# Kernel tuning notes

Measured on AMD Instinct MI355X. Metric: run time of the kernel, lower is better.

## Reference

```python
import jax, jax.numpy as jnp
import numpy as np

CODEBOOK_SIZE = 8192
EMBED_DIM = 128
BETA = 0.25


def setup_inputs() -> dict:
    key = jax.random.key(0)
    k1, k2, k3, k4 = jax.random.split(key, 4)
    z = jax.random.normal(k1, (8, 4096, EMBED_DIM), dtype=jnp.float32)
    # nn.Embedding init: normal(0, D**-0.5), frozen
    emb_weight = jax.random.normal(k2, (CODEBOOK_SIZE, EMBED_DIM), dtype=jnp.float32) * (EMBED_DIM ** -0.5)
    # nn.Linear default init scale ~ 1/sqrt(in_features)
    lim = 1.0 / np.sqrt(EMBED_DIM)
    proj_w = jax.random.uniform(k3, (EMBED_DIM, EMBED_DIM), jnp.float32, -lim, lim)
    proj_b = jax.random.uniform(k4, (EMBED_DIM,), jnp.float32, -lim, lim)
    return {"z": z, "emb_weight": emb_weight, "proj_w": proj_w, "proj_b": proj_b}


def reference(z, emb_weight, proj_w, proj_b):
    z_flat = z.reshape(-1, EMBED_DIM)  # [T, D]
    # embedding_proj: Linear -> codebook @ W^T + b
    quant_codebook = emb_weight @ proj_w.T + proj_b  # [K, D]
    # squared distances: |z|^2 + |c|^2 - 2 z c^T  -> [T, K]
    d = (jnp.sum(z_flat ** 2, axis=1, keepdims=True)
         + jnp.sum(quant_codebook ** 2, axis=1)
         - 2.0 * jnp.einsum('td,kd->tk', z_flat, quant_codebook))
    idx = jnp.argmin(d, axis=1)  # [T]
    z_q = quant_codebook[idx].reshape(z.shape)
    # codebook usage / perplexity
    counts = jax.ops.segment_sum(jnp.ones_like(idx, dtype=jnp.float32), idx,
                                 num_segments=CODEBOOK_SIZE)
    e_mean = counts / idx.shape[0]
    perplexity = jnp.exp(-jnp.sum(e_mean * jnp.log(e_mean + 1e-8)))
    sg = jax.lax.stop_gradient
    commit_loss = (BETA * jnp.mean((sg(z_q) - z) ** 2)
                   + jnp.mean((z_q - sg(z)) ** 2))
    z_q_st = z + sg(z_q - z)  # straight-through estimator
    return (z_q_st, commit_loss, perplexity)
```

## Files before the change

kernel.cpp:

```cpp
#include <hip/hip_runtime.h>
#include <math.h>

#define T_TOK 32768
#define D_DIM 128
#define K_CODE 8192
#define BM 256
#define BN 64

typedef unsigned long long ull;
typedef _Float16 v8h __attribute__((ext_vector_type(8)));
typedef _Float16 v4h __attribute__((ext_vector_type(4)));
typedef float v16f __attribute__((ext_vector_type(16)));

#define SCALE 4096.0f
#define DESCALE (1.0f / 4096.0f)
#define ACC_SCALE (-0x1p-23f)


__global__ __launch_bounds__(64) void proj_kernel(const float* __restrict__ E,
                                                  const float* __restrict__ W,
                                                  const float* __restrict__ b,
                                                  char* __restrict__ Cpack,
                                                  float* __restrict__ cn) {
    int r = blockIdx.x;
    int l = threadIdx.x;
    const float4* E4 = (const float4*)(E + (size_t)r * D_DIM);
    const float4* WA = (const float4*)(W + (size_t)l * D_DIM);
    const float4* WB = (const float4*)(W + (size_t)(l + 64) * D_DIM);

    float4 aA = make_float4(0.f, 0.f, 0.f, 0.f);
    float4 aB = make_float4(0.f, 0.f, 0.f, 0.f);
#pragma unroll
    for (int dd = 0; dd < 32; ++dd) {
        float4 e = E4[dd];
        float4 wa = WA[dd], wb = WB[dd];
        aA.x = fmaf(e.x, wa.x, aA.x);
        aA.y = fmaf(e.y, wa.y, aA.y);
        aA.z = fmaf(e.z, wa.z, aA.z);
        aA.w = fmaf(e.w, wa.w, aA.w);
        aB.x = fmaf(e.x, wb.x, aB.x);
        aB.y = fmaf(e.y, wb.y, aB.y);
        aB.z = fmaf(e.z, wb.z, aB.z);
        aB.w = fmaf(e.w, wb.w, aB.w);
    }
    float vA = ((aA.x + aA.y) + (aA.z + aA.w)) + b[l];
    float vB = ((aB.x + aB.y) + (aB.z + aB.w)) + b[l + 64];

    char* cp = Cpack + (size_t)(r >> 6) * 32768;
    int mt = (r >> 5) & 1, rs = r & 31;
    {
        int kc = l >> 4, hf = (l >> 3) & 1, j = l & 7;
        float f = vA * SCALE;
        _Float16 h = (_Float16)f;
        _Float16 m = (_Float16)(f - (float)h);
        size_t off = (size_t)((mt * 8 + kc) * 1024 + (hf * 32 + rs) * 16 + j * 2);
        *(_Float16*)(cp + off) = h;
        *(_Float16*)(cp + off + 16384) = m;
    }
    {
        int d = l + 64;
        int kc = d >> 4, hf = (d >> 3) & 1, j = d & 7;
        float f = vB * SCALE;
        _Float16 h = (_Float16)f;
        _Float16 m = (_Float16)(f - (float)h);
        size_t off = (size_t)((mt * 8 + kc) * 1024 + (hf * 32 + rs) * 16 + j * 2);
        *(_Float16*)(cp + off) = h;
        *(_Float16*)(cp + off + 16384) = m;
    }

    float s = vA * vA + vB * vB;
#pragma unroll
    for (int off = 32; off > 0; off >>= 1) s += __shfl_down(s, off, 64);
    if (l == 0) cn[r] = s;
}

__global__ __launch_bounds__(64) void znorm_kernel(const float* __restrict__ Z,
                                                   float* __restrict__ zn,
                                                   ull* __restrict__ packed,
                                                   int* __restrict__ counts,
                                                   float* __restrict__ loss) {
    int t = blockIdx.x;
    int l = threadIdx.x;
    float a = Z[(size_t)t * D_DIM + l];
    float b2 = Z[(size_t)t * D_DIM + 64 + l];
    float s = a * a + b2 * b2;
#pragma unroll
    for (int off = 32; off > 0; off >>= 1) s += __shfl_down(s, off, 64);
    if (l == 0) {
        zn[t] = s;
        packed[t] = ~0ull;
        if (t < K_CODE) counts[t] = 0;
        if (t == 0) loss[0] = 0.f;
    }
}

__global__ __launch_bounds__(256) void prep_z_kernel(const float* __restrict__ Z,
                                                     char* __restrict__ Zpack) {
    int tb = blockIdx.x;
    int tid = threadIdx.x;
    int lane = tid & 63;
    int w = tid >> 6;
    char* zp = Zpack + (size_t)tb * 16384;
#pragma unroll
    for (int kq = 0; kq < 2; ++kq) {
        int kc = 2 * w + kq;
        const float* src = Z + (size_t)(tb * 32 + (lane & 31)) * D_DIM
                             + kc * 16 + (lane >> 5) * 8;
        float4 a = *(const float4*)(src);
        float4 c = *(const float4*)(src + 4);
        float vals[8] = {a.x, a.y, a.z, a.w, c.x, c.y, c.z, c.w};
        v8h h, m;
#pragma unroll
        for (int j = 0; j < 8; ++j) {
            float f = vals[j] * SCALE;
            _Float16 hh = (_Float16)f;
            h[j] = hh;
            m[j] = (_Float16)(f - (float)hh);
        }
        *(v8h*)(zp + (size_t)(kc * 1024 + lane * 16)) = h;
        *(v8h*)(zp + (size_t)(8192 + kc * 1024 + lane * 16)) = m;
    }
}

__global__ __launch_bounds__(256, 3) void argmin_kernel(const char* __restrict__ Zpack,
                                                        const char* __restrict__ Cpack,
                                                        const float* __restrict__ cn,
                                                        const float* __restrict__ zn,
                                                        ull* __restrict__ packed) {
    __shared__ char lds[33024];

    int tid = threadIdx.x;
    int lane = tid & 63;
    int w = __builtin_amdgcn_readfirstlane(tid >> 6);
    int cb = blockIdx.x;
    int nb = cb * BN;
    int mb = blockIdx.y * BM;

    {
        const float4* src = (const float4*)(Cpack + (size_t)cb * 32768);
        float4* dst = (float4*)lds;
#pragma unroll
        for (int it = 0; it < 8; ++it) dst[it * 256 + tid] = src[it * 256 + tid];
        if (tid < 64) *(float*)(lds + 32768 + tid * 4) = cn[nb + tid];
    }
    __syncthreads();

    v16f acc[2][2];
#pragma unroll
    for (int mt = 0; mt < 2; ++mt)
#pragma unroll
        for (int nt = 0; nt < 2; ++nt) acc[mt][nt] = (v16f)0.f;

    int tb0 = (mb >> 5) + 2 * w;
    const char* zb00 = Zpack + (size_t)tb0 * 16384 + lane * 16;
    const char* zb01 = zb00 + 8192;
    const char* zb10 = Zpack + (size_t)(tb0 + 1) * 16384 + lane * 16;
    const char* zb11 = zb10 + 8192;
    const char* ab = lds + lane * 16;

    v8h pBh0 = *(const v8h*)(zb00);
    v8h pBm0 = *(const v8h*)(zb01);
    v8h pBh1 = *(const v8h*)(zb10);
    v8h pBm1 = *(const v8h*)(zb11);

#pragma unroll
    for (int kc = 0; kc < 8; ++kc) {
        v8h Bh0 = pBh0, Bm0 = pBm0, Bh1 = pBh1, Bm1 = pBm1;
        if (kc < 7) {
            pBh0 = *(const v8h*)(zb00 + (kc + 1) * 1024);
            pBm0 = *(const v8h*)(zb01 + (kc + 1) * 1024);
            pBh1 = *(const v8h*)(zb10 + (kc + 1) * 1024);
            pBm1 = *(const v8h*)(zb11 + (kc + 1) * 1024);
        }
        v8h Ah0 = *(const v8h*)(ab + (0 * 8 + kc) * 1024);
        v8h Ah1 = *(const v8h*)(ab + (1 * 8 + kc) * 1024);
        v8h Am0 = *(const v8h*)(ab + (2 * 8 + kc) * 1024);
        v8h Am1 = *(const v8h*)(ab + (3 * 8 + kc) * 1024);

        acc[0][0] = __builtin_amdgcn_mfma_f32_32x32x16_f16(Ah0, Bh0, acc[0][0], 0, 0, 0);
        acc[0][1] = __builtin_amdgcn_mfma_f32_32x32x16_f16(Ah0, Bh1, acc[0][1], 0, 0, 0);
        acc[1][0] = __builtin_amdgcn_mfma_f32_32x32x16_f16(Ah1, Bh0, acc[1][0], 0, 0, 0);
        acc[1][1] = __builtin_amdgcn_mfma_f32_32x32x16_f16(Ah1, Bh1, acc[1][1], 0, 0, 0);
        acc[0][0] = __builtin_amdgcn_mfma_f32_32x32x16_f16(Ah0, Bm0, acc[0][0], 0, 0, 0);
        acc[0][1] = __builtin_amdgcn_mfma_f32_32x32x16_f16(Ah0, Bm1, acc[0][1], 0, 0, 0);
        acc[1][0] = __builtin_amdgcn_mfma_f32_32x32x16_f16(Ah1, Bm0, acc[1][0], 0, 0, 0);
        acc[1][1] = __builtin_amdgcn_mfma_f32_32x32x16_f16(Ah1, Bm1, acc[1][1], 0, 0, 0);
        acc[0][0] = __builtin_amdgcn_mfma_f32_32x32x16_f16(Am0, Bh0, acc[0][0], 0, 0, 0);
        acc[0][1] = __builtin_amdgcn_mfma_f32_32x32x16_f16(Am0, Bh1, acc[0][1], 0, 0, 0);
        acc[1][0] = __builtin_amdgcn_mfma_f32_32x32x16_f16(Am1, Bh0, acc[1][0], 0, 0, 0);
        acc[1][1] = __builtin_amdgcn_mfma_f32_32x32x16_f16(Am1, Bh1, acc[1][1], 0, 0, 0);
    }

    const float* cn_s = (const float*)(lds + 32768);
    int half_id = lane >> 5;
    int tok0 = mb + w * 64 + (lane & 31);
    int tok1 = tok0 + 32;
    float zn0 = zn[tok0], zn1 = zn[tok1];

    float best0 = 3.4e38f, best1 = 3.4e38f;
    int bi0 = nb, bi1 = nb;
#pragma unroll
    for (int mt = 0; mt < 2; ++mt) {
#pragma unroll
        for (int reg = 0; reg < 16; ++reg) {
            int mrow = 32 * mt + (reg & 3) + 8 * (reg >> 2) + 4 * half_id;
            float cnv = cn_s[mrow];
            int code = nb + mrow;
            float s0 = fmaf(acc[mt][0][reg], ACC_SCALE, zn0 + cnv);
            float s1 = fmaf(acc[mt][1][reg], ACC_SCALE, zn1 + cnv);
            if (s0 < best0) { best0 = s0; bi0 = code; }
            if (s1 < best1) { best1 = s1; bi1 = code; }
        }
    }
    {
        float ob = __shfl_xor(best0, 32, 64);
        int oi = __shfl_xor(bi0, 32, 64);
        if (ob < best0 || (ob == best0 && oi < bi0)) { best0 = ob; bi0 = oi; }
        ob = __shfl_xor(best1, 32, 64);
        oi = __shfl_xor(bi1, 32, 64);
        if (ob < best1 || (ob == best1 && oi < bi1)) { best1 = ob; bi1 = oi; }
    }
    if (half_id == 0) {
        ull pk = ((ull)__float_as_uint(best0) << 32) | (unsigned)bi0;
        atomicMin(&packed[tok0], pk);
    } else {
        ull pk = ((ull)__float_as_uint(best1) << 32) | (unsigned)bi1;
        atomicMin(&packed[tok1], pk);
    }
}

__global__ __launch_bounds__(256) void zq_kernel(const float* __restrict__ Z,
                                                 const char* __restrict__ Cpack,
                                                 const ull* __restrict__ packed,
                                                 float* __restrict__ out,
                                                 int* __restrict__ counts,
                                                 float* __restrict__ loss) {
    int gid = blockIdx.x * 256 + threadIdx.x;
    int t = gid >> 5;
    int d4 = gid & 31;
    int idx = (int)(packed[t] & 0xFFFFFFFFull);
    if (d4 == 0) atomicAdd(&counts[idx], 1);

    int d0 = 4 * d4;
    int kc = d0 >> 4, hf = (d0 >> 3) & 1, j0 = d0 & 7;
    const char* cp = Cpack + (size_t)(idx >> 6) * 32768
                   + (size_t)((((idx >> 5) & 1) * 8 + kc) * 1024
                              + (hf * 32 + (idx & 31)) * 16 + j0 * 2);
    v4h h = *(const v4h*)(cp);
    v4h m = *(const v4h*)(cp + 16384);
    float4 cv;
    cv.x = ((float)h[0] + (float)m[0]) * DESCALE;
    cv.y = ((float)h[1] + (float)m[1]) * DESCALE;
    cv.z = ((float)h[2] + (float)m[2]) * DESCALE;
    cv.w = ((float)h[3] + (float)m[3]) * DESCALE;

    float4 zv = ((const float4*)Z)[gid];
    float dx = cv.x - zv.x, dy = cv.y - zv.y, dz = cv.z - zv.z, dw = cv.w - zv.w;
    float4 o;
    o.x = zv.x + dx;
    o.y = zv.y + dy;
    o.z = zv.z + dz;
    o.w = zv.w + dw;
    ((float4*)out)[gid] = o;

    float ls = dx * dx + dy * dy + dz * dz + dw * dw;
#pragma unroll
    for (int off = 32; off > 0; off >>= 1) ls += __shfl_down(ls, off, 64);
    __shared__ float red[4];
    int lane = threadIdx.x & 63, w = threadIdx.x >> 6;
    if (lane == 0) red[w] = ls;
    __syncthreads();
    if (threadIdx.x == 0) {
        atomicAdd(loss, (red[0] + red[1]) + (red[2] + red[3]));
    }
}

__global__ __launch_bounds__(256) void scalars_kernel(const int* __restrict__ counts,
                                                      const float* __restrict__ loss,
                                                      float* __restrict__ out) {
    float s = 0.f;
    for (int i = threadIdx.x; i < K_CODE; i += 256) {
        float e = (float)counts[i] * (1.0f / (float)T_TOK);
        s += e * logf(e + 1e-8f);
    }
#pragma unroll
    for (int off = 32; off > 0; off >>= 1) s += __shfl_down(s, off, 64);
    __shared__ float red[4];
    int lane = threadIdx.x & 63, w = threadIdx.x >> 6;
    if (lane == 0) red[w] = s;
    __syncthreads();
    if (threadIdx.x == 0) {
        float ssum = (red[0] + red[1]) + (red[2] + red[3]);
        out[(size_t)T_TOK * D_DIM + 0] = 1.25f * loss[0] / (float)((size_t)T_TOK * D_DIM);
        out[(size_t)T_TOK * D_DIM + 1] = expf(-ssum);
    }
}

extern "C" void kernel_launch(void* const* d_in, const int* in_sizes, int n_in,
                              void* d_out, int out_size, void* d_ws, size_t ws_size,
                              hipStream_t stream) {
    const float* z   = (const float*)d_in[0];
    const float* emb = (const float*)d_in[1];
    const float* pw  = (const float*)d_in[2];
    const float* pb  = (const float*)d_in[3];
    float* out = (float*)d_out;

    char* Zpack = (char*)d_out;

    char* ws = (char*)d_ws;
    char*  Cpack  = ws + 0;
    float* cn     = (float*)(ws + 4194304);
    float* zn     = (float*)(ws + 4227072);
    ull*   packed = (ull*)  (ws + 4358144);
    int*   counts = (int*)  (ws + 4620288);
    float* loss   = (float*)(ws + 4653056);

    proj_kernel<<<K_CODE, 64, 0, stream>>>(emb, pw, pb, Cpack, cn);
    prep_z_kernel<<<T_TOK / 32, 256, 0, stream>>>(z, Zpack);
    znorm_kernel<<<T_TOK, 64, 0, stream>>>(z, zn, packed, counts, loss);
    argmin_kernel<<<dim3(K_CODE / BN, T_TOK / BM), 256, 0, stream>>>(Zpack, Cpack, cn, zn, packed);
    zq_kernel<<<(T_TOK * D_DIM / 4) / 256, 256, 0, stream>>>(z, Cpack, packed, out, counts, loss);
    scalars_kernel<<<1, 256, 0, stream>>>(counts, loss, out);
}
```

Measured before the change: 419.9 us.

## Fuse prep kernels into one launch and double-buffer argmin operand loads

Merges the codebook projection, Z packing and Z norm/init kernels into a single prep launch split by block index, removing two kernel launches and their gaps. The argmin kernel now uses two-deep register rings, fetching B from global two k-steps ahead and prefetching A from LDS one step ahead. This is meant to hide global and LDS load latency behind the MFMAs, at the cost of more VGPRs, which could reduce occupancy under the 3-block launch bound.

```diff
diff --git a/kernel.cpp b/kernel.cpp
--- a/kernel.cpp
+++ b/kernel.cpp
@@ -17,108 +17,110 @@
 #define ACC_SCALE (-0x1p-23f)
 
 
-__global__ __launch_bounds__(64) void proj_kernel(const float* __restrict__ E,
-                                                  const float* __restrict__ W,
-                                                  const float* __restrict__ b,
-                                                  char* __restrict__ Cpack,
-                                                  float* __restrict__ cn) {
-    int r = blockIdx.x;
-    int l = threadIdx.x;
-    const float4* E4 = (const float4*)(E + (size_t)r * D_DIM);
-    const float4* WA = (const float4*)(W + (size_t)l * D_DIM);
-    const float4* WB = (const float4*)(W + (size_t)(l + 64) * D_DIM);
-
-    float4 aA = make_float4(0.f, 0.f, 0.f, 0.f);
-    float4 aB = make_float4(0.f, 0.f, 0.f, 0.f);
-#pragma unroll
-    for (int dd = 0; dd < 32; ++dd) {
-        float4 e = E4[dd];
-        float4 wa = WA[dd], wb = WB[dd];
-        aA.x = fmaf(e.x, wa.x, aA.x);
-        aA.y = fmaf(e.y, wa.y, aA.y);
-        aA.z = fmaf(e.z, wa.z, aA.z);
-        aA.w = fmaf(e.w, wa.w, aA.w);
-        aB.x = fmaf(e.x, wb.x, aB.x);
-        aB.y = fmaf(e.y, wb.y, aB.y);
-        aB.z = fmaf(e.z, wb.z, aB.z);
-        aB.w = fmaf(e.w, wb.w, aB.w);
-    }
-    float vA = ((aA.x + aA.y) + (aA.z + aA.w)) + b[l];
-    float vB = ((aB.x + aB.y) + (aB.z + aB.w)) + b[l + 64];
-
-    char* cp = Cpack + (size_t)(r >> 6) * 32768;
-    int mt = (r >> 5) & 1, rs = r & 31;
-    {
-        int kc = l >> 4, hf = (l >> 3) & 1, j = l & 7;
-        float f = vA * SCALE;
-        _Float16 h = (_Float16)f;
-        _Float16 m = (_Float16)(f - (float)h);
-        size_t off = (size_t)((mt * 8 + kc) * 1024 + (hf * 32 + rs) * 16 + j * 2);
-        *(_Float16*)(cp + off) = h;
-        *(_Float16*)(cp + off + 16384) = m;
-    }
-    {
-        int d = l + 64;
-        int kc = d >> 4, hf = (d >> 3) & 1, j = d & 7;
-        float f = vB * SCALE;
-        _Float16 h = (_Float16)f;
-        _Float16 m = (_Float16)(f - (float)h);
-        size_t off = (size_t)((mt * 8 + kc) * 1024 + (hf * 32 + rs) * 16 + j * 2);
-        *(_Float16*)(cp + off) = h;
-        *(_Float16*)(cp + off + 16384) = m;
-    }
-
-    float s = vA * vA + vB * vB;
-#pragma unroll
-    for (int off = 32; off > 0; off >>= 1) s += __shfl_down(s, off, 64);
-    if (l == 0) cn[r] = s;
-}
-
-__global__ __launch_bounds__(64) void znorm_kernel(const float* __restrict__ Z,
+__global__ __launch_bounds__(256) void prep_kernel(const float* __restrict__ E,
+                                                   const float* __restrict__ W,
+                                                   const float* __restrict__ b,
+                                                   const float* __restrict__ Z,
+                                                   char* __restrict__ Cpack,
+                                                   float* __restrict__ cn,
+                                                   char* __restrict__ Zpack,
                                                    float* __restrict__ zn,
                                                    ull* __restrict__ packed,
                                                    int* __restrict__ counts,
                                                    float* __restrict__ loss) {
-    int t = blockIdx.x;
-    int l = threadIdx.x;
-    float a = Z[(size_t)t * D_DIM + l];
-    float b2 = Z[(size_t)t * D_DIM + 64 + l];
-    float s = a * a + b2 * b2;
-#pragma unroll
-    for (int off = 32; off > 0; off >>= 1) s += __shfl_down(s, off, 64);
-    if (l == 0) {
-        zn[t] = s;
-        packed[t] = ~0ull;
-        if (t < K_CODE) counts[t] = 0;
-        if (t == 0) loss[0] = 0.f;
-    }
-}
-
-__global__ __launch_bounds__(256) void prep_z_kernel(const float* __restrict__ Z,
-                                                     char* __restrict__ Zpack) {
-    int tb = blockIdx.x;
+    int bid = blockIdx.x;
     int tid = threadIdx.x;
     int lane = tid & 63;
     int w = tid >> 6;
-    char* zp = Zpack + (size_t)tb * 16384;
-#pragma unroll
-    for (int kq = 0; kq < 2; ++kq) {
-        int kc = 2 * w + kq;
-        const float* src = Z + (size_t)(tb * 32 + (lane & 31)) * D_DIM
-                             + kc * 16 + (lane >> 5) * 8;
-        float4 a = *(const float4*)(src);
-        float4 c = *(const float4*)(src + 4);
-        float vals[8] = {a.x, a.y, a.z, a.w, c.x, c.y, c.z, c.w};
-        v8h h, m;
-#pragma unroll
-        for (int j = 0; j < 8; ++j) {
-            float f = vals[j] * SCALE;
-            _Float16 hh = (_Float16)f;
-            h[j] = hh;
-            m[j] = (_Float16)(f - (float)hh);
-        }
-        *(v8h*)(zp + (size_t)(kc * 1024 + lane * 16)) = h;
-        *(v8h*)(zp + (size_t)(8192 + kc * 1024 + lane * 16)) = m;
+
+    if (bid < 2048) {
+        int r = bid * 4 + w;
+        int l = lane;
+        const float4* E4 = (const float4*)(E + (size_t)r * D_DIM);
+        const float4* WA = (const float4*)(W + (size_t)l * D_DIM);
+        const float4* WB = (const float4*)(W + (size_t)(l + 64) * D_DIM);
+
+        float4 aA = make_float4(0.f, 0.f, 0.f, 0.f);
+        float4 aB = make_float4(0.f, 0.f, 0.f, 0.f);
+#pragma unroll
+        for (int dd = 0; dd < 32; ++dd) {
+            float4 e = E4[dd];
+            float4 wa = WA[dd], wb = WB[dd];
+            aA.x = fmaf(e.x, wa.x, aA.x);
+            aA.y = fmaf(e.y, wa.y, aA.y);
+            aA.z = fmaf(e.z, wa.z, aA.z);
+            aA.w = fmaf(e.w, wa.w, aA.w);
+            aB.x = fmaf(e.x, wb.x, aB.x);
+            aB.y = fmaf(e.y, wb.y, aB.y);
+            aB.z = fmaf(e.z, wb.z, aB.z);
+            aB.w = fmaf(e.w, wb.w, aB.w);
+        }
+        float vA = ((aA.x + aA.y) + (aA.z + aA.w)) + b[l];
+        float vB = ((aB.x + aB.y) + (aB.z + aB.w)) + b[l + 64];
+
+        char* cp = Cpack + (size_t)(r >> 6) * 32768;
+        int mt = (r >> 5) & 1, rs = r & 31;
+        {
+            int kc = l >> 4, hf = (l >> 3) & 1, j = l & 7;
+            float f = vA * SCALE;
+            _Float16 h = (_Float16)f;
+            _Float16 m = (_Float16)(f - (float)h);
+            size_t off = (size_t)((mt * 8 + kc) * 1024 + (hf * 32 + rs) * 16 + j * 2);
+            *(_Float16*)(cp + off) = h;
+            *(_Float16*)(cp + off + 16384) = m;
+        }
+        {
+            int d = l + 64;
+            int kc = d >> 4, hf = (d >> 3) & 1, j = d & 7;
+            float f = vB * SCALE;
+            _Float16 h = (_Float16)f;
+            _Float16 m = (_Float16)(f - (float)h);
+            size_t off = (size_t)((mt * 8 + kc) * 1024 + (hf * 32 + rs) * 16 + j * 2);
+            *(_Float16*)(cp + off) = h;
+            *(_Float16*)(cp + off + 16384) = m;
+        }
+
+        float s = vA * vA + vB * vB;
+#pragma unroll
+        for (int off = 32; off > 0; off >>= 1) s += __shfl_down(s, off, 64);
+        if (l == 0) cn[r] = s;
+    } else {
+        int tb = bid - 2048;
+        char* zp = Zpack + (size_t)tb * 16384;
+#pragma unroll
+        for (int kq = 0; kq < 2; ++kq) {
+            int kc = 2 * w + kq;
+            const float* src = Z + (size_t)(tb * 32 + (lane & 31)) * D_DIM
+                                 + kc * 16 + (lane >> 5) * 8;
+            float4 a = *(const float4*)(src);
+            float4 c = *(const float4*)(src + 4);
+            float vals[8] = {a.x, a.y, a.z, a.w, c.x, c.y, c.z, c.w};
+            v8h h, m;
+#pragma unroll
+            for (int j = 0; j < 8; ++j) {
+                float f = vals[j] * SCALE;
+                _Float16 hh = (_Float16)f;
+                h[j] = hh;
+                m[j] = (_Float16)(f - (float)hh);
+            }
+            *(v8h*)(zp + (size_t)(kc * 1024 + lane * 16)) = h;
+            *(v8h*)(zp + (size_t)(8192 + kc * 1024 + lane * 16)) = m;
+        }
+#pragma unroll
+        for (int i = 0; i < 8; ++i) {
+            int t = tb * 32 + 8 * w + i;
+            float a = Z[(size_t)t * D_DIM + lane];
+            float b2 = Z[(size_t)t * D_DIM + 64 + lane];
+            float s = a * a + b2 * b2;
+#pragma unroll
+            for (int off = 32; off > 0; off >>= 1) s += __shfl_down(s, off, 64);
+            if (lane == 0) {
+                zn[t] = s;
+                packed[t] = ~0ull;
+            }
+        }
+        if (tb < 32) counts[tb * 256 + tid] = 0;
+        if (tb == 32 && tid == 0) loss[0] = 0.f;
     }
 }
 
@@ -158,24 +160,40 @@
     const char* zb11 = zb10 + 8192;
     const char* ab = lds + lane * 16;
 
-    v8h pBh0 = *(const v8h*)(zb00);
-    v8h pBm0 = *(const v8h*)(zb01);
-    v8h pBh1 = *(const v8h*)(zb10);
-    v8h pBm1 = *(const v8h*)(zb11);
+    v8h Bring[2][4];
+    Bring[0][0] = *(const v8h*)(zb00);
+    Bring[0][1] = *(const v8h*)(zb01);
+    Bring[0][2] = *(const v8h*)(zb10);
+    Bring[0][3] = *(const v8h*)(zb11);
+    Bring[1][0] = *(const v8h*)(zb00 + 1024);
+    Bring[1][1] = *(const v8h*)(zb01 + 1024);
+    Bring[1][2] = *(const v8h*)(zb10 + 1024);
+    Bring[1][3] = *(const v8h*)(zb11 + 1024);
+
+    v8h Aring[2][4];
+#pragma unroll
+    for (int s = 0; s < 4; ++s) Aring[0][s] = *(const v8h*)(ab + (s * 8) * 1024);
 
 #pragma unroll
     for (int kc = 0; kc < 8; ++kc) {
-        v8h Bh0 = pBh0, Bm0 = pBm0, Bh1 = pBh1, Bm1 = pBm1;
+        const int cur = kc & 1;
+        const int nxt = cur ^ 1;
+        v8h Ah0 = Aring[cur][0], Ah1 = Aring[cur][1];
+        v8h Am0 = Aring[cur][2], Am1 = Aring[cur][3];
+        v8h Bh0 = Bring[cur][0], Bm0 = Bring[cur][1];
+        v8h Bh1 = Bring[cur][2], Bm1 = Bring[cur][3];
+
         if (kc < 7) {
-            pBh0 = *(const v8h*)(zb00 + (kc + 1) * 1024);
-            pBm0 = *(const v8h*)(zb01 + (kc + 1) * 1024);
-            pBh1 = *(const v8h*)(zb10 + (kc + 1) * 1024);
-            pBm1 = *(const v8h*)(zb11 + (kc + 1) * 1024);
-        }
-        v8h Ah0 = *(const v8h*)(ab + (0 * 8 + kc) * 1024);
-        v8h Ah1 = *(const v8h*)(ab + (1 * 8 + kc) * 1024);
-        v8h Am0 = *(const v8h*)(ab + (2 * 8 + kc) * 1024);
-        v8h Am1 = *(const v8h*)(ab + (3 * 8 + kc) * 1024);
+#pragma unroll
+            for (int s = 0; s < 4; ++s)
+                Aring[nxt][s] = *(const v8h*)(ab + (s * 8 + kc + 1) * 1024);
+        }
+        if (kc < 6) {
+            Bring[cur][0] = *(const v8h*)(zb00 + (kc + 2) * 1024);
+            Bring[cur][1] = *(const v8h*)(zb01 + (kc + 2) * 1024);
+            Bring[cur][2] = *(const v8h*)(zb10 + (kc + 2) * 1024);
+            Bring[cur][3] = *(const v8h*)(zb11 + (kc + 2) * 1024);
+        }
 
         acc[0][0] = __builtin_amdgcn_mfma_f32_32x32x16_f16(Ah0, Bh0, acc[0][0], 0, 0, 0);
         acc[0][1] = __builtin_amdgcn_mfma_f32_32x32x16_f16(Ah0, Bh1, acc[0][1], 0, 0, 0);
@@ -315,9 +333,8 @@
     int*   counts = (int*)  (ws + 4620288);
     float* loss   = (float*)(ws + 4653056);
 
-    proj_kernel<<<K_CODE, 64, 0, stream>>>(emb, pw, pb, Cpack, cn);
-    prep_z_kernel<<<T_TOK / 32, 256, 0, stream>>>(z, Zpack);
-    znorm_kernel<<<T_TOK, 64, 0, stream>>>(z, zn, packed, counts, loss);
+    prep_kernel<<<3072, 256, 0, stream>>>(emb, pw, pb, z, Cpack, cn, Zpack, zn,
+                                          packed, counts, loss);
     argmin_kernel<<<dim3(K_CODE / BN, T_TOK / BM), 256, 0, stream>>>(Zpack, Cpack, cn, zn, packed);
     zq_kernel<<<(T_TOK * D_DIM / 4) / 256, 256, 0, stream>>>(z, Cpack, packed, out, counts, loss);
     scalars_kernel<<<1, 256, 0, stream>>>(counts, loss, out);
```

New measurement: 436.7 us. +4.0%, slower.
